# Kernel optimization log

Measured on AMD Instinct MI355X. Metric: run time of the kernel, lower is better.

The kernel has to match this reference:

```python
import jax, jax.numpy as jnp
import numpy as np

B, S, HID = 1, 2048, 2048
N_HEADS = 16
HEAD_DIM = HID // N_HEADS  # 128
ROPE_THETA = 10000.0
NEG_INF = -1e9


def setup_inputs() -> dict:
    key = jax.random.key(0)
    ks = jax.random.split(key, 5)
    hidden_states = jax.random.normal(ks[0], (B, S, HID), dtype=jnp.float32)
    scale = 1.0 / np.sqrt(HID)
    Wq = jax.random.normal(ks[1], (HID, HID), dtype=jnp.float32) * scale
    Wk = jax.random.normal(ks[2], (HID, HID), dtype=jnp.float32) * scale
    Wv = jax.random.normal(ks[3], (HID, HID), dtype=jnp.float32) * scale
    Wo = jax.random.normal(ks[4], (HID, HID), dtype=jnp.float32) * scale
    # additive causal mask [B, 1, S, S]: 0 on/below diag, -1e9 above
    causal = jnp.tril(jnp.ones((S, S), dtype=bool))
    attention_mask = jnp.where(causal, 0.0, NEG_INF).astype(jnp.float32)[None, None]
    attention_mask = jnp.broadcast_to(attention_mask, (B, 1, S, S))
    position_ids = jnp.broadcast_to(jnp.arange(S, dtype=jnp.int64)[None, :], (B, S))
    return {"hidden_states": hidden_states, "Wq": Wq, "Wk": Wk, "Wv": Wv,
            "Wo": Wo, "attention_mask": attention_mask, "position_ids": position_ids}


def _rotate_half(x):
    x1, x2 = jnp.split(x, 2, axis=-1)
    return jnp.concatenate((-x2, x1), axis=-1)


def _rope_cos_sin(position_ids, head_dim, dtype):
    inv_freq = 1.0 / (ROPE_THETA ** (jnp.arange(0, head_dim, 2, dtype=jnp.float32) / head_dim))
    freqs = position_ids.astype(jnp.float32)[:, :, None] * inv_freq[None, None, :]  # [b, s, d/2]
    emb = jnp.concatenate((freqs, freqs), axis=-1)  # [b, s, d]
    # unsqueeze_dim=1 -> broadcast over heads
    return jnp.cos(emb).astype(dtype)[:, None], jnp.sin(emb).astype(dtype)[:, None]


def reference(hidden_states, Wq, Wk, Wv, Wo, attention_mask, position_ids):
    b, s, h = hidden_states.shape
    d = HEAD_DIM
    def proj(W):
        return (hidden_states @ W.T).reshape(b, s, N_HEADS, d).transpose(0, 2, 1, 3)  # [b,h,s,d]
    q, k, v = proj(Wq), proj(Wk), proj(Wv)
    cos, sin = _rope_cos_sin(position_ids, d, q.dtype)
    q = q * cos + _rotate_half(q) * sin
    k = k * cos + _rotate_half(k) * sin
    scores = jnp.einsum('bhqd,bhkd->bhqk', q, k) / jnp.sqrt(jnp.float32(d))
    scores = scores + attention_mask
    probs = jax.nn.softmax(scores.astype(jnp.float32), axis=-1).astype(q.dtype)
    attn = jnp.einsum('bhqk,bhkd->bhqd', probs, v)
    out = attn.transpose(0, 2, 1, 3).reshape(b, s, h)
    return out @ Wo.T
```

## Files before the change

### kernel.cpp

```cpp
#include <hip/hip_runtime.h>

typedef _Float16 half8 __attribute__((ext_vector_type(8)));
typedef _Float16 half4 __attribute__((ext_vector_type(4)));
typedef float floatx4 __attribute__((ext_vector_type(4)));
typedef float floatx16 __attribute__((ext_vector_type(16)));

#define GLDS(gp, lp) __builtin_amdgcn_global_load_lds( \
    (const __attribute__((address_space(1))) void*)(gp), \
    (__attribute__((address_space(3))) void*)(lp), 16, 0, 0)

__global__ void cvt_f2h5(const float* __restrict__ s0, const float* __restrict__ s1,
                         const float* __restrict__ s2, const float* __restrict__ s3,
                         const float* __restrict__ s4,
                         _Float16* __restrict__ d0, _Float16* __restrict__ d1,
                         _Float16* __restrict__ d2, _Float16* __restrict__ d3,
                         _Float16* __restrict__ d4, int n8) {
  int i = blockIdx.x * 256 + threadIdx.x;
  if (i >= n8) return;
  const float* s; _Float16* d;
  switch (blockIdx.y) {
    case 0: s = s0; d = d0; break;
    case 1: s = s1; d = d1; break;
    case 2: s = s2; d = d2; break;
    case 3: s = s3; d = d3; break;
    default: s = s4; d = d4; break;
  }
  const float4* s4p = (const float4*)s;
  float4 a = s4p[2 * i], b = s4p[2 * i + 1];
  half8 h;
  h[0] = (_Float16)a.x; h[1] = (_Float16)a.y; h[2] = (_Float16)a.z; h[3] = (_Float16)a.w;
  h[4] = (_Float16)b.x; h[5] = (_Float16)b.y; h[6] = (_Float16)b.z; h[7] = (_Float16)b.w;
  *(half8*)(d + 8 * (size_t)i) = h;
}

__global__ __launch_bounds__(256) void transpose_k(const _Float16* __restrict__ src,
                                                   _Float16* __restrict__ dst) {
  __shared__ _Float16 t[64][72];
  const int r0 = blockIdx.y * 64, c0 = blockIdx.x * 64;
  const int tr = threadIdx.x >> 3, tc = (threadIdx.x & 7) * 8;
  #pragma unroll
  for (int p = 0; p < 2; ++p) {
    half8 v = *(const half8*)(src + (size_t)(r0 + p * 32 + tr) * 2048 + c0 + tc);
    *(half8*)&t[p * 32 + tr][tc] = v;
  }
  __syncthreads();
  #pragma unroll
  for (int p = 0; p < 2; ++p) {
    half8 v;
    #pragma unroll
    for (int j = 0; j < 8; ++j) v[j] = t[tc + j][p * 32 + tr];
    *(half8*)(dst + (size_t)(c0 + p * 32 + tr) * 2048 + r0 + tc) = v;
  }
}

template <int OUTF>
__global__ __launch_bounds__(512, 2) void gemm8(const _Float16* __restrict__ A,
                                                const _Float16* __restrict__ B,
                                                _Float16* __restrict__ Ch,
                                                float* __restrict__ Cf,
                                                long long bStride, long long cStride) {
  extern __shared__ _Float16 lds[];
  _Float16* As = lds;
  _Float16* Bs = lds + 4 * 8192;

  const int tid = threadIdx.x, lane = tid & 63, wv = tid >> 6;
  const int fr = lane & 15, fg = lane >> 4;
  const int wm = wv >> 2, wn = wv & 3;
  const int bm = blockIdx.y * 256, bn = blockIdx.x * 256;
  const _Float16* Ab = A + (size_t)bm * 2048;
  const _Float16* Bb = B + (size_t)blockIdx.z * bStride + (size_t)bn * 2048;

  const int srow = lane >> 2;
  const int gsw = (lane & 3) ^ ((srow >> 1) & 3);
  const int asw = (fr >> 1) & 3;

  auto stageA = [&](int t) {
    const int kc = t * 32;
    _Float16* dst = As + (t & 3) * 8192;
    #pragma unroll
    for (int g = 0; g < 2; ++g) {
      const int rb = wv * 32 + g * 16;
      GLDS(Ab + (size_t)(rb + srow) * 2048 + kc + gsw * 8, dst + rb * 32);
    }
  };
  auto stageB = [&](int t) {
    const int kc = t * 32;
    _Float16* dst = Bs + (t & 3) * 8192;
    #pragma unroll
    for (int g = 0; g < 2; ++g) {
      const int rb = wv * 32 + g * 16;
      GLDS(Bb + (size_t)(rb + srow) * 2048 + kc + gsw * 8, dst + rb * 32);
    }
  };

  floatx4 acc[8][4] = {};

  stageA(0); stageB(0);
  stageA(1); stageB(1);
  stageA(2); stageB(2);

  for (int t = 0; t < 64; ++t) {
    const _Float16* Ac = As + (t & 3) * 8192;
    const _Float16* Bc = Bs + (t & 3) * 8192;
    if (t + 3 < 64) stageA(t + 3);
    const int rem = 63 - t;
    if (rem >= 3)      asm volatile("s_waitcnt vmcnt(10)" ::: "memory");
    else if (rem == 2) asm volatile("s_waitcnt vmcnt(8)" ::: "memory");
    else if (rem == 1) asm volatile("s_waitcnt vmcnt(4)" ::: "memory");
    else               asm volatile("s_waitcnt vmcnt(0)" ::: "memory");
    __builtin_amdgcn_s_barrier();

    half8 bf[4], af[4];
    #pragma unroll
    for (int n = 0; n < 4; ++n)
      bf[n] = *(const half8*)(Bc + (wn * 64 + n * 16 + fr) * 32 + ((fg ^ asw) * 8));
    #pragma unroll
    for (int m = 0; m < 4; ++m)
      af[m] = *(const half8*)(Ac + (wm * 128 + m * 16 + fr) * 32 + ((fg ^ asw) * 8));
    asm volatile("s_waitcnt lgkmcnt(0)" ::: "memory");
    __builtin_amdgcn_sched_barrier(0);
    __builtin_amdgcn_s_setprio(1);
    #pragma unroll
    for (int m = 0; m < 4; ++m)
      #pragma unroll
      for (int n = 0; n < 4; ++n)
        acc[m][n] = __builtin_amdgcn_mfma_f32_16x16x32_f16(af[m], bf[n], acc[m][n], 0, 0, 0);
    __builtin_amdgcn_s_setprio(0);
    __builtin_amdgcn_s_barrier();

    if (t + 3 < 64) stageB(t + 3);
    #pragma unroll
    for (int m = 0; m < 4; ++m)
      af[m] = *(const half8*)(Ac + (wm * 128 + 64 + m * 16 + fr) * 32 + ((fg ^ asw) * 8));
    asm volatile("s_waitcnt lgkmcnt(0)" ::: "memory");
    __builtin_amdgcn_sched_barrier(0);
    __builtin_amdgcn_s_setprio(1);
    #pragma unroll
    for (int m = 0; m < 4; ++m)
      #pragma unroll
      for (int n = 0; n < 4; ++n)
        acc[m + 4][n] = __builtin_amdgcn_mfma_f32_16x16x32_f16(af[m], bf[n], acc[m + 4][n], 0, 0, 0);
    __builtin_amdgcn_s_setprio(0);
    __builtin_amdgcn_s_barrier();
  }

  #pragma unroll
  for (int m = 0; m < 8; ++m)
    #pragma unroll
    for (int n = 0; n < 4; ++n)
      #pragma unroll
      for (int i = 0; i < 4; ++i) {
        const int row = bm + wm * 128 + m * 16 + fg * 4 + i;
        const int col = bn + wn * 64 + n * 16 + fr;
        if (OUTF)
          Cf[(size_t)row * 2048 + col] = acc[m][n][i];
        else
          Ch[(size_t)blockIdx.z * cStride + (size_t)row * 2048 + col] = (_Float16)acc[m][n][i];
      }
}

template <int OUTF, int BN>
__global__ __launch_bounds__(256) void gemm_nt(const _Float16* __restrict__ A,
                                               const _Float16* __restrict__ B,
                                               _Float16* __restrict__ Ch,
                                               float* __restrict__ Cf,
                                               long long bStride, long long cStride) {
  __shared__ _Float16 As[2][128 * 32];
  __shared__ _Float16 Bs[2][BN * 32];
  const int NF = BN / 32;
  const int tid = threadIdx.x, lane = tid & 63, wv = tid >> 6;
  const int fr = lane & 15, fg = lane >> 4;
  const int bm = blockIdx.y * 128, bn = blockIdx.x * BN;
  const _Float16* Ab = A + (size_t)bm * 2048;
  const _Float16* Bb = B + (size_t)blockIdx.z * bStride + (size_t)bn * 2048;
  const int srow = lane >> 2;
  const int gsw = (lane & 3) ^ ((lane >> 3) & 3);
  const int asw = (fr >> 1) & 3;

  floatx4 acc[4][NF] = {};

  auto stage = [&](int buf, int kt) {
    #pragma unroll
    for (int r = 0; r < 2; ++r) {
      int row = r * 64 + wv * 16 + srow;
      GLDS(Ab + (size_t)row * 2048 + kt * 32 + gsw * 8, &As[buf][(r * 64 + wv * 16) * 32]);
    }
    #pragma unroll
    for (int r = 0; r < BN / 64; ++r) {
      int row = r * 64 + wv * 16 + srow;
      GLDS(Bb + (size_t)row * 2048 + kt * 32 + gsw * 8, &Bs[buf][(r * 64 + wv * 16) * 32]);
    }
  };
  const int wm = (wv >> 1) * 64, wn = (wv & 1) * (BN / 2);

  stage(0, 0);
  __syncthreads();

  #pragma unroll 2
  for (int kt = 0; kt < 64; ++kt) {
    const int cur = kt & 1;
    if (kt < 63) stage(cur ^ 1, kt + 1);
    half8 af[4], bf[NF];
    #pragma unroll
    for (int m = 0; m < 4; ++m)
      af[m] = *(const half8*)&As[cur][(wm + m * 16 + fr) * 32 + ((fg ^ asw) * 8)];
    #pragma unroll
    for (int n = 0; n < NF; ++n)
      bf[n] = *(const half8*)&Bs[cur][(wn + n * 16 + fr) * 32 + ((fg ^ asw) * 8)];
    #pragma unroll
    for (int m = 0; m < 4; ++m)
      #pragma unroll
      for (int n = 0; n < NF; ++n)
        acc[m][n] = __builtin_amdgcn_mfma_f32_16x16x32_f16(af[m], bf[n], acc[m][n], 0, 0, 0);
    __syncthreads();
  }

  #pragma unroll
  for (int m = 0; m < 4; ++m)
    #pragma unroll
    for (int n = 0; n < NF; ++n)
      #pragma unroll
      for (int i = 0; i < 4; ++i) {
        const int row = bm + wm + m * 16 + fg * 4 + i;
        const int col = bn + wn + n * 16 + fr;
        if (OUTF)
          Cf[(size_t)row * 2048 + col] = acc[m][n][i];
        else
          Ch[(size_t)blockIdx.z * cStride + (size_t)row * 2048 + col] = (_Float16)acc[m][n][i];
      }
}

__global__ void rope_k(_Float16* __restrict__ Q, _Float16* __restrict__ K) {
  const int idx = blockIdx.x * 256 + threadIdx.x;
  const int s = idx >> 10;
  const int hd = idx & 1023;
  const int head = hd >> 6, d = hd & 63;
  const float freq = powf(10000.0f, -(float)d * (1.0f / 64.0f));
  const float ang = (float)s * freq;
  float sn, c;
  sincosf(ang, &sn, &c);
  const size_t base = (size_t)s * 2048 + head * 128 + d;
  float q1 = (float)Q[base], q2 = (float)Q[base + 64];
  Q[base]      = (_Float16)(q1 * c - q2 * sn);
  Q[base + 64] = (_Float16)(q2 * c + q1 * sn);
  float k1 = (float)K[base], k2 = (float)K[base + 64];
  K[base]      = (_Float16)(k1 * c - k2 * sn);
  K[base + 64] = (_Float16)(k2 * c + k1 * sn);
}

__global__ __launch_bounds__(256, 2) void attn_k(const _Float16* __restrict__ Qp,
                                                 const _Float16* __restrict__ Kp,
                                                 const _Float16* __restrict__ Vt,
                                                 _Float16* __restrict__ Po,
                                                 float* __restrict__ Pr) {
  extern __shared__ _Float16 smem[];
  _Float16* Ks = smem;
  _Float16* Vs = smem + 2 * 64 * 128;
  _Float16* Pb = smem + 4 * 64 * 128;

  const int tid = threadIdx.x, lane = tid & 63, wv = tid >> 6;
  const int l31 = lane & 31, hi = lane >> 5;
  const int wq = wv >> 1, wk = wv & 1;

  const int bid = (int)blockIdx.x;
  const int head = ((bid & 7) << 1) | ((bid >> 3) & 1);
  const int L = bid >> 4;
  int g, it0, itEnd;
  if (L < 16) { g = 16 + L; it0 = 0; itEnd = 16; }
  else {
    const int j = (L - 16) >> 1;
    if ((L & 1) == 0) { g = 15 - j; it0 = 0; itEnd = g + 1; }
    else             { g = 31 - j; it0 = 16; itEnd = g + 1; }
  }
  const size_t hoff = (size_t)head * 128;
  const int qw = g * 64 + wq * 32;
  _Float16* Pw = Pb + wv * (32 * 40);

  half8 qf[8];
  const _Float16 scl = (_Float16)0.08838834764831845f;
  #pragma unroll
  for (int ks = 0; ks < 8; ++ks) {
    half8 t = *(const half8*)(Qp + (size_t)(qw + l31) * 2048 + hoff + ks * 16 + hi * 8);
    #pragma unroll
    for (int j = 0; j < 8; ++j) t[j] = (_Float16)(t[j] * scl);
    qf[ks] = t;
  }

  auto stage = [&](int buf, int it) {
    const int kv0 = it * 64;
    #pragma unroll
    for (int i = 0; i < 4; ++i) {
      const int rbase = wv * 16 + i * 4;
      const int row = rbase + (lane >> 4);
      const int gr = (lane & 15) ^ (row & 7);
      GLDS(Kp + (size_t)(kv0 + row) * 2048 + hoff + gr * 8,
           Ks + buf * 8192 + rbase * 128);
    }
    #pragma unroll
    for (int i = 0; i < 4; ++i) {
      const int rbase = wv * 32 + i * 8;
      const int row = rbase + (lane >> 3);
      const int gr = (lane & 7) ^ (row & 7);
      GLDS(Vt + (size_t)(hoff + row) * 2048 + kv0 + gr * 8,
           Vs + buf * 8192 + rbase * 64);
    }
  };

  floatx16 o[4] = {};
  float rsum = 0.0f;

  stage(0, it0);
  __syncthreads();

  int buf = 0;
  for (int it = it0; it < itEnd; ++it) {
    if (it + 1 < itEnd) stage(buf ^ 1, it + 1);
    const _Float16* Kb = Ks + buf * 8192;
    const _Float16* Vb = Vs + buf * 8192;

    const int krow = wk * 32 + l31;
    const int ksw = l31 & 7;
    floatx16 S = {};
    __builtin_amdgcn_s_setprio(1);
    #pragma unroll
    for (int ks = 0; ks < 8; ++ks) {
      half8 a = *(const half8*)(Kb + krow * 128 + (((ks * 2 + hi) ^ ksw) * 8));
      S = __builtin_amdgcn_mfma_f32_32x32x16_f16(a, qf[ks], S, 0, 0, 0);
    }
    __builtin_amdgcn_s_setprio(0);

    if (it == g) {
      const int kv0 = it * 64;
      const int qa = qw + l31;
      #pragma unroll
      for (int r = 0; r < 16; ++r) {
        const int ka = kv0 + wk * 32 + (r & 3) + 8 * (r >> 2) + 4 * hi;
        if (ka > qa) S[r] = -1e30f;
      }
    }

    #pragma unroll
    for (int r4 = 0; r4 < 4; ++r4) {
      float p0 = __expf(S[4 * r4 + 0] - 8.0f);
      float p1 = __expf(S[4 * r4 + 1] - 8.0f);
      float p2 = __expf(S[4 * r4 + 2] - 8.0f);
      float p3 = __expf(S[4 * r4 + 3] - 8.0f);
      rsum += (p0 + p1) + (p2 + p3);
      half4 pk;
      pk[0] = (_Float16)p0; pk[1] = (_Float16)p1;
      pk[2] = (_Float16)p2; pk[3] = (_Float16)p3;
      *(half4*)(Pw + l31 * 40 + r4 * 8 + hi * 4) = pk;
    }

    half8 pa0 = *(const half8*)(Pw + l31 * 40 + hi * 8);
    half8 pa1 = *(const half8*)(Pw + l31 * 40 + 16 + hi * 8);

    __builtin_amdgcn_s_setprio(1);
    #pragma unroll
    for (int dt = 0; dt < 4; ++dt) {
      const int vrow = dt * 32 + l31;
      const int vsw = vrow & 7;
      half8 b0 = *(const half8*)(Vb + vrow * 64 + (((wk * 4 + hi) ^ vsw) * 8));
      half8 b1 = *(const half8*)(Vb + vrow * 64 + (((wk * 4 + 2 + hi) ^ vsw) * 8));
      o[dt] = __builtin_amdgcn_mfma_f32_32x32x16_f16(pa0, b0, o[dt], 0, 0, 0);
      o[dt] = __builtin_amdgcn_mfma_f32_32x32x16_f16(pa1, b1, o[dt], 0, 0, 0);
    }
    __builtin_amdgcn_s_setprio(0);

    __syncthreads();
    buf ^= 1;
  }

  float* Mo = (float*)smem;
  float* Mr = (float*)(smem + 16384);
  if (wk == 1) {
    #pragma unroll
    for (int dt = 0; dt < 4; ++dt)
      #pragma unroll
      for (int r = 0; r < 16; ++r)
        Mo[((wq * 4 + dt) * 16 + r) * 64 + lane] = o[dt][r];
    Mr[wq * 64 + lane] = rsum;
  }
  __syncthreads();
  if (wk == 0) {
    rsum += Mr[wq * 64 + lane];
    float rs = rsum;
    rs += __shfl_xor(rs, 32);
    if (hi == 0) Pr[(size_t)bid * 64 + wq * 32 + l31] = rs;
    #pragma unroll
    for (int dt = 0; dt < 4; ++dt)
      #pragma unroll
      for (int r = 0; r < 16; ++r) {
        const float w = o[dt][r] + Mo[((wq * 4 + dt) * 16 + r) * 64 + lane];
        const int ql = wq * 32 + (r & 3) + 8 * (r >> 2) + 4 * hi;
        Po[(size_t)bid * 8192 + ql * 128 + dt * 32 + l31] = (_Float16)w;
      }
  }
}

__global__ __launch_bounds__(256) void attn_merge(const _Float16* __restrict__ Po,
                                                  const float* __restrict__ Pr,
                                                  _Float16* __restrict__ At) {
  const int bidx = (int)blockIdx.x;
  const int h = bidx & 15, g = bidx >> 4;
  const int hb = ((h & 1) << 3) | (h >> 1);
  const int L0 = (g >= 16) ? (g - 16) : (16 + 2 * (15 - g));
  const int U0 = L0 * 16 + hb;
  const bool two = (g >= 16);
  const int U1 = two ? ((17 + 2 * (31 - g)) * 16 + hb) : 0;
  const int t = threadIdx.x;
  const int q = t >> 2, cs = t & 3;
  const float r0 = Pr[(size_t)U0 * 64 + q];
  const float r1 = two ? Pr[(size_t)U1 * 64 + q] : 0.0f;
  const float inv = 1.0f / (r0 + r1);
  const size_t orow = (size_t)(g * 64 + q) * 2048 + h * 128;
  #pragma unroll
  for (int s = 0; s < 4; ++s) {
    const int d0 = (cs + s * 4) * 8;
    half8 a = *(const half8*)(Po + (size_t)U0 * 8192 + q * 128 + d0);
    half8 o;
    if (two) {
      half8 b = *(const half8*)(Po + (size_t)U1 * 8192 + q * 128 + d0);
      #pragma unroll
      for (int j = 0; j < 8; ++j) o[j] = (_Float16)(((float)a[j] + (float)b[j]) * inv);
    } else {
      #pragma unroll
      for (int j = 0; j < 8; ++j) o[j] = (_Float16)((float)a[j] * inv);
    }
    *(half8*)(At + orow + d0) = o;
  }
}

extern "C" void kernel_launch(void* const* d_in, const int* in_sizes, int n_in,
                              void* d_out, int out_size, void* d_ws, size_t ws_size,
                              hipStream_t stream) {
  (void)in_sizes; (void)n_in; (void)out_size; (void)ws_size;
  const float* X  = (const float*)d_in[0];
  const float* Wq = (const float*)d_in[1];
  const float* Wk = (const float*)d_in[2];
  const float* Wv = (const float*)d_in[3];
  const float* Wo = (const float*)d_in[4];
  float* out = (float*)d_out;

  const size_t SZ = 2048ull * 2048ull;
  _Float16* ws  = (_Float16*)d_ws;
  _Float16* Xh  = ws + 0 * SZ;
  _Float16* Wqh = ws + 1 * SZ;
  _Float16* Wkh = ws + 2 * SZ;
  _Float16* Wvh = ws + 3 * SZ;
  _Float16* Woh = ws + 4 * SZ;
  _Float16* Qp  = ws + 5 * SZ;
  _Float16* Kp  = ws + 6 * SZ;
  _Float16* Vp  = ws + 7 * SZ;
  _Float16* Vtg = Wqh;
  _Float16* At  = Xh;
  _Float16* Po  = Wkh;
  float*    Pr  = (float*)Vp;

  const int n8 = (int)(SZ / 8);
  dim3 blk(256);

  cvt_f2h5<<<dim3(n8 / 256, 5), blk, 0, stream>>>(X, Wq, Wk, Wv, Wo,
                                                  Xh, Wqh, Wkh, Wvh, Woh, n8);

  gemm8<0><<<dim3(8, 8, 3), dim3(512), 131072, stream>>>(Xh, Wqh, Qp, nullptr,
                                                         (long long)SZ, (long long)SZ);
  rope_k<<<(2048 * 1024) / 256, blk, 0, stream>>>(Qp, Kp);
  transpose_k<<<dim3(32, 32), blk, 0, stream>>>(Vp, Vtg);

  const size_t attn_lds = (4 * 64 * 128 + 4 * 32 * 40) * sizeof(_Float16);
  attn_k<<<768, blk, attn_lds, stream>>>(Qp, Kp, Vtg, Po, Pr);
  attn_merge<<<512, blk, 0, stream>>>(Po, Pr, At);

  gemm_nt<1, 64><<<dim3(32, 16, 1), blk, 0, stream>>>(At, Woh, nullptr, out, 0, 0);
}
```

Before: 174.9 us.

## Restructure gemm8 mainloop to double-buffered 64-wide K tiles with quadrant scheduling

The projection GEMM kernel moves from a 4-stage ring of 32-wide K tiles to a 2-stage double buffer of 64-wide K tiles, with a new XOR swizzle over 8 chunks. Each K step is split into four quadrant phases that interleave LDS fragment reads, prefetch of the next tile, and MFMA bursts. This halves the number of outer iterations and barrier rounds per K, but the shallower prefetch depth and a vmcnt(0) wait inside each step may expose more global-memory latency.

Result: no change. 174.9 us (+0.0%).

```diff
diff --git a/kernel.cpp b/kernel.cpp
--- a/kernel.cpp
+++ b/kernel.cpp
@@ -61,7 +61,7 @@
                                                 long long bStride, long long cStride) {
   extern __shared__ _Float16 lds[];
   _Float16* As = lds;
-  _Float16* Bs = lds + 4 * 8192;
+  _Float16* Bs = lds + 2 * 16384;
 
   const int tid = threadIdx.x, lane = tid & 63, wv = tid >> 6;
   const int fr = lane & 15, fg = lane >> 4;
@@ -70,78 +70,83 @@
   const _Float16* Ab = A + (size_t)bm * 2048;
   const _Float16* Bb = B + (size_t)blockIdx.z * bStride + (size_t)bn * 2048;
 
-  const int srow = lane >> 2;
-  const int gsw = (lane & 3) ^ ((srow >> 1) & 3);
-  const int asw = (fr >> 1) & 3;
-
-  auto stageA = [&](int t) {
-    const int kc = t * 32;
-    _Float16* dst = As + (t & 3) * 8192;
+  const int srow = lane >> 3;
+  const int sgr = (lane & 7) ^ srow;
+
+  auto stageA = [&](int t, int h) {
+    _Float16* dst = As + (t & 1) * 16384;
+    const size_t coff = (size_t)t * 64 + sgr * 8;
     #pragma unroll
     for (int g = 0; g < 2; ++g) {
-      const int rb = wv * 32 + g * 16;
-      GLDS(Ab + (size_t)(rb + srow) * 2048 + kc + gsw * 8, dst + rb * 32);
+      const int rb = h * 128 + wv * 16 + g * 8;
+      GLDS(Ab + (size_t)(rb + srow) * 2048 + coff, dst + rb * 64);
     }
   };
-  auto stageB = [&](int t) {
-    const int kc = t * 32;
-    _Float16* dst = Bs + (t & 3) * 8192;
+  auto stageB = [&](int t, int h) {
+    _Float16* dst = Bs + (t & 1) * 16384;
+    const size_t coff = (size_t)t * 64 + sgr * 8;
     #pragma unroll
     for (int g = 0; g < 2; ++g) {
-      const int rb = wv * 32 + g * 16;
-      GLDS(Bb + (size_t)(rb + srow) * 2048 + kc + gsw * 8, dst + rb * 32);
+      const int rb = h * 128 + wv * 16 + g * 8;
+      GLDS(Bb + (size_t)(rb + srow) * 2048 + coff, dst + rb * 64);
     }
   };
 
+  const int arow = wm * 128 + fr;
+  const int brow = wn * 64 + fr;
+  const int sl0 = ((fg) ^ (fr & 7)) * 8;
+  const int sl1 = ((4 + fg) ^ (fr & 7)) * 8;
+
   floatx4 acc[8][4] = {};
 
-  stageA(0); stageB(0);
-  stageA(1); stageB(1);
-  stageA(2); stageB(2);
-
-  for (int t = 0; t < 64; ++t) {
-    const _Float16* Ac = As + (t & 3) * 8192;
-    const _Float16* Bc = Bs + (t & 3) * 8192;
-    if (t + 3 < 64) stageA(t + 3);
-    const int rem = 63 - t;
-    if (rem >= 3)      asm volatile("s_waitcnt vmcnt(10)" ::: "memory");
-    else if (rem == 2) asm volatile("s_waitcnt vmcnt(8)" ::: "memory");
-    else if (rem == 1) asm volatile("s_waitcnt vmcnt(4)" ::: "memory");
-    else               asm volatile("s_waitcnt vmcnt(0)" ::: "memory");
-    __builtin_amdgcn_s_barrier();
-
-    half8 bf[4], af[4];
-    #pragma unroll
-    for (int n = 0; n < 4; ++n)
-      bf[n] = *(const half8*)(Bc + (wn * 64 + n * 16 + fr) * 32 + ((fg ^ asw) * 8));
-    #pragma unroll
-    for (int m = 0; m < 4; ++m)
-      af[m] = *(const half8*)(Ac + (wm * 128 + m * 16 + fr) * 32 + ((fg ^ asw) * 8));
-    asm volatile("s_waitcnt lgkmcnt(0)" ::: "memory");
-    __builtin_amdgcn_sched_barrier(0);
-    __builtin_amdgcn_s_setprio(1);
-    #pragma unroll
-    for (int m = 0; m < 4; ++m)
-      #pragma unroll
-      for (int n = 0; n < 4; ++n)
-        acc[m][n] = __builtin_amdgcn_mfma_f32_16x16x32_f16(af[m], bf[n], acc[m][n], 0, 0, 0);
-    __builtin_amdgcn_s_setprio(0);
-    __builtin_amdgcn_s_barrier();
-
-    if (t + 3 < 64) stageB(t + 3);
-    #pragma unroll
-    for (int m = 0; m < 4; ++m)
-      af[m] = *(const half8*)(Ac + (wm * 128 + 64 + m * 16 + fr) * 32 + ((fg ^ asw) * 8));
-    asm volatile("s_waitcnt lgkmcnt(0)" ::: "memory");
-    __builtin_amdgcn_sched_barrier(0);
-    __builtin_amdgcn_s_setprio(1);
-    #pragma unroll
-    for (int m = 0; m < 4; ++m)
-      #pragma unroll
-      for (int n = 0; n < 4; ++n)
-        acc[m + 4][n] = __builtin_amdgcn_mfma_f32_16x16x32_f16(af[m], bf[n], acc[m + 4][n], 0, 0, 0);
-    __builtin_amdgcn_s_setprio(0);
-    __builtin_amdgcn_s_barrier();
+  stageA(0, 0); stageA(0, 1); stageB(0, 0); stageB(0, 1);
+  asm volatile("s_waitcnt vmcnt(0)" ::: "memory");
+  __builtin_amdgcn_s_barrier();
+
+  for (int t = 0; t < 32; ++t) {
+    const _Float16* Ac = As + (t & 1) * 16384;
+    const _Float16* Bc = Bs + (t & 1) * 16384;
+    half8 af[4][2], bf[2][2];
+    #pragma unroll
+    for (int p = 0; p < 4; ++p) {
+      const int qm = p >> 1, qn = p & 1;
+      if (qn == 0) {
+        #pragma unroll
+        for (int m = 0; m < 4; ++m) {
+          const int r = arow + qm * 64 + m * 16;
+          af[m][0] = *(const half8*)(Ac + r * 64 + sl0);
+          af[m][1] = *(const half8*)(Ac + r * 64 + sl1);
+        }
+      }
+      #pragma unroll
+      for (int n = 0; n < 2; ++n) {
+        const int r = brow + qn * 32 + n * 16;
+        bf[n][0] = *(const half8*)(Bc + r * 64 + sl0);
+        bf[n][1] = *(const half8*)(Bc + r * 64 + sl1);
+      }
+      if (t + 1 < 32) {
+        if (p == 0) { stageA(t + 1, 0); stageA(t + 1, 1); }
+        else if (p == 1) { stageB(t + 1, 0); stageB(t + 1, 1); }
+      }
+      __builtin_amdgcn_s_barrier();
+      asm volatile("s_waitcnt lgkmcnt(0)" ::: "memory");
+      __builtin_amdgcn_sched_barrier(0);
+      __builtin_amdgcn_s_setprio(1);
+      #pragma unroll
+      for (int m = 0; m < 4; ++m)
+        #pragma unroll
+        for (int n = 0; n < 2; ++n) {
+          acc[qm * 4 + m][qn * 2 + n] =
+              __builtin_amdgcn_mfma_f32_16x16x32_f16(af[m][0], bf[n][0],
+                                                     acc[qm * 4 + m][qn * 2 + n], 0, 0, 0);
+          acc[qm * 4 + m][qn * 2 + n] =
+              __builtin_amdgcn_mfma_f32_16x16x32_f16(af[m][1], bf[n][1],
+                                                     acc[qm * 4 + m][qn * 2 + n], 0, 0, 0);
+        }
+      __builtin_amdgcn_s_setprio(0);
+      if (p == 2) asm volatile("s_waitcnt vmcnt(0)" ::: "memory");
+      __builtin_amdgcn_s_barrier();
+    }
   }
 
   #pragma unroll
```
